# Performance work log

Hardware: AMD Instinct MI355X
Metric: run time of the kernel (lower is better)

Reference implementation:

```python
import jax, jax.numpy as jnp
import numpy as np

B, T, U, D, H, V = 2, 512, 128, 512, 512, 1024

def setup_inputs() -> dict:
    key = jax.random.key(0)
    k1, k2, k3, k4 = jax.random.split(key, 4)
    pred_inp = jax.random.normal(k1, (B, U, D), dtype=jnp.float32)
    enc_inp = jax.random.normal(k2, (B, T, D), dtype=jnp.float32)
    W0 = jax.random.normal(k3, (D, H), dtype=jnp.float32) * (1.0 / np.sqrt(D))
    b0 = jnp.zeros((H,), dtype=jnp.float32)
    W1 = jax.random.normal(k4, (H, V), dtype=jnp.float32) * (1.0 / np.sqrt(H))
    b1 = jnp.zeros((V,), dtype=jnp.float32)
    return {"pred_inp": pred_inp, "enc_inp": enc_inp, "W0": W0, "b0": b0, "W1": W1, "b1": b1}

def reference(pred_inp, enc_inp, W0, b0, W1, b1):
    # broadcast-add: enc [B,T,1,D] + pred [B,1,U,D] -> [B,T,U,D]
    x = enc_inp[:, :, None, :] + pred_inp[:, None, :, :]
    # Dense(additional_size)
    h = jnp.einsum('btud,dh->btuh', x, W0) + b0
    # Dense(output_size)
    out = jnp.einsum('btuh,hv->btuv', h, W1) + b1
    return out
```

## Files before the change

kernel.cpp:

```cpp
#include <hip/hip_runtime.h>


typedef float vf4 __attribute__((ext_vector_type(4)));
typedef short bf16x8 __attribute__((ext_vector_type(8)));
typedef float f32x4 __attribute__((ext_vector_type(4)));
typedef unsigned short us4 __attribute__((ext_vector_type(4)));

#define PADK 40

__device__ __forceinline__ unsigned short f2bf(float f) {
    union { float f; unsigned u; } v; v.f = f;
    const unsigned r = v.u + 0x7FFFu + ((v.u >> 16) & 1u);
    return (unsigned short)(r >> 16);
}

__global__ __launch_bounds__(256) void prep(
    const float* __restrict__ pred, const float* __restrict__ enc,
    const float* __restrict__ W0, const float* __restrict__ b0,
    const float* __restrict__ W1, const float* __restrict__ b1,
    unsigned short* __restrict__ xbf,
    unsigned short* __restrict__ WcT,
    float* __restrict__ bcv)
{
    __shared__ unsigned short As[64 * PADK];
    __shared__ unsigned short Bst[64 * PADK];
    __shared__ float b0s[512];

    const int bid = blockIdx.x;
    const int tid = threadIdx.x;

    if (bid < 128) {
        const int row0 = (bid >> 4) << 6;
        const int col0 = (bid & 15) << 6;
        const int w = tid >> 6, lane = tid & 63;
        const int l16 = lane & 15, kq = lane >> 4;

        float4 ar[2], br[2];
        auto loadA = [&](int kb) {
            #pragma unroll
            for (int i = 0; i < 2; ++i) {
                const int idx = tid + (i << 8);
                const int r = idx >> 3, k4 = (idx & 7) << 2;
                ar[i] = *reinterpret_cast<const float4*>(
                    W0 + (size_t)(row0 + r) * 512 + kb + k4);
            }
        };
        auto loadB = [&](int kb) {
            #pragma unroll
            for (int i = 0; i < 2; ++i) {
                const int idx = tid + (i << 8);
                const int kk = idx >> 4, n4 = (idx & 15) << 2;
                br[i] = *reinterpret_cast<const float4*>(
                    W1 + (size_t)(kb + kk) * 1024 + col0 + n4);
            }
        };
        auto stage = [&]() {
            #pragma unroll
            for (int i = 0; i < 2; ++i) {
                const int idx = tid + (i << 8);
                const int r = idx >> 3, k4 = (idx & 7) << 2;
                us4 p = { f2bf(ar[i].x), f2bf(ar[i].y), f2bf(ar[i].z), f2bf(ar[i].w) };
                *reinterpret_cast<us4*>(&As[r * PADK + k4]) = p;
                const int kk = idx >> 4, n4 = (idx & 15) << 2;
                Bst[(n4 + 0) * PADK + kk] = f2bf(br[i].x);
                Bst[(n4 + 1) * PADK + kk] = f2bf(br[i].y);
                Bst[(n4 + 2) * PADK + kk] = f2bf(br[i].z);
                Bst[(n4 + 3) * PADK + kk] = f2bf(br[i].w);
            }
        };

        f32x4 acc[4] = {};
        loadA(0); loadB(0);
        for (int kt = 0; kt < 16; ++kt) {
            __syncthreads();
            stage();
            __syncthreads();
            if (kt < 15) { loadA((kt + 1) << 5); loadB((kt + 1) << 5); }
            bf16x8 a = *reinterpret_cast<const bf16x8*>(&As[(w * 16 + l16) * PADK + kq * 8]);
            #pragma unroll
            for (int nf = 0; nf < 4; ++nf) {
                bf16x8 b = *reinterpret_cast<const bf16x8*>(&Bst[(nf * 16 + l16) * PADK + kq * 8]);
                acc[nf] = __builtin_amdgcn_mfma_f32_16x16x32_bf16(a, b, acc[nf], 0, 0, 0);
            }
        }
        const int cr0 = row0 + w * 16 + kq * 4;
        #pragma unroll
        for (int nf = 0; nf < 4; ++nf) {
            const int c = col0 + nf * 16 + l16;
            us4 p = { f2bf(acc[nf][0]), f2bf(acc[nf][1]),
                      f2bf(acc[nf][2]), f2bf(acc[nf][3]) };
            *reinterpret_cast<us4*>(&WcT[(size_t)c * 512 + cr0]) = p;
        }
    } else if (bid < 448) {
        const int i = ((bid - 128) << 8) + tid;
        const int r = i >> 6;
        const int k8 = (i & 63) << 3;
        const float* src = (r < 1024)
            ? enc + (size_t)r * 512 + k8
            : pred + (size_t)(r - 1024) * 512 + k8;
        const float4 a = *reinterpret_cast<const float4*>(src);
        const float4 c = *reinterpret_cast<const float4*>(src + 4);
        us4 p0 = { f2bf(a.x), f2bf(a.y), f2bf(a.z), f2bf(a.w) };
        us4 p1 = { f2bf(c.x), f2bf(c.y), f2bf(c.z), f2bf(c.w) };
        *reinterpret_cast<us4*>(&xbf[(size_t)r * 512 + k8]) = p0;
        *reinterpret_cast<us4*>(&xbf[(size_t)r * 512 + k8 + 4]) = p1;
    } else {
        for (int i = tid; i < 512; i += 256) b0s[i] = b0[i];
        __syncthreads();
        const int v = ((bid - 448) << 8) + tid;
        float acc = b1[v];
        #pragma unroll 8
        for (int h = 0; h < 512; ++h)
            acc = fmaf(b0s[h], W1[(size_t)h * 1024 + v], acc);
        bcv[v] = acc;
    }
}

__global__ __launch_bounds__(256) void gemm_y(
    const unsigned short* __restrict__ xbf,
    const unsigned short* __restrict__ WcT,
    const float* __restrict__ bcv,
    float* __restrict__ Q)
{
    __shared__ unsigned short As[2][64 * PADK];
    __shared__ unsigned short Bs[2][64 * PADK];

    const int tid = threadIdx.x;
    const int row0 = blockIdx.y << 6;
    const int col0 = blockIdx.x << 6;
    const int w = tid >> 6, lane = tid & 63;
    const int l16 = lane & 15, kq = lane >> 4;
    const int sr = tid >> 2, sk8 = (tid & 3) << 3;

    const unsigned short* Arow = xbf + (size_t)(row0 + sr) * 512 + sk8;
    const unsigned short* Brow = WcT + (size_t)(col0 + sr) * 512 + sk8;

    bf16x8 areg, breg;
    auto loadg = [&](int kb) {
        areg = *reinterpret_cast<const bf16x8*>(Arow + kb);
        breg = *reinterpret_cast<const bf16x8*>(Brow + kb);
    };
    auto stage = [&](int buf) {
        *reinterpret_cast<bf16x8*>(&As[buf][sr * PADK + sk8]) = areg;
        *reinterpret_cast<bf16x8*>(&Bs[buf][sr * PADK + sk8]) = breg;
    };

    f32x4 acc[4] = {};
    loadg(0);
    stage(0);
    __syncthreads();
    int buf = 0;
    for (int kt = 0; kt < 16; ++kt) {
        if (kt < 15) loadg((kt + 1) << 5);
        bf16x8 a = *reinterpret_cast<const bf16x8*>(&As[buf][(w * 16 + l16) * PADK + kq * 8]);
        #pragma unroll
        for (int nf = 0; nf < 4; ++nf) {
            bf16x8 b = *reinterpret_cast<const bf16x8*>(&Bs[buf][(nf * 16 + l16) * PADK + kq * 8]);
            acc[nf] = __builtin_amdgcn_mfma_f32_16x16x32_bf16(a, b, acc[nf], 0, 0, 0);
        }
        if (kt < 15) stage(buf ^ 1);
        __syncthreads();
        buf ^= 1;
    }

    const int cr0 = row0 + w * 16 + kq * 4;
    const bool doBias = (row0 >= 1024);
    #pragma unroll
    for (int nf = 0; nf < 4; ++nf) {
        const int c = col0 + nf * 16 + l16;
        const float bv = doBias ? bcv[c] : 0.0f;
        #pragma unroll
        for (int r = 0; r < 4; ++r)
            Q[(size_t)(cr0 + r) * 1024 + c] = acc[nf][r] + bv;
    }
}

__global__ __launch_bounds__(256) void bcast_add(
    const vf4* __restrict__ Q, vf4* __restrict__ out)
{
    const int bid = blockIdx.x;
    const int g   = bid >> 4;
    const int uh  = (bid >> 3) & 1;
    const int vt  = bid & 7;
    const int bt0 = g << 3;
    const int b   = bt0 >> 9;
    const int u8  = threadIdx.x >> 5;
    const int c4  = threadIdx.x & 31;
    const int vcol = vt * 32 + c4;

    vf4 ye[8], yp[8];
    #pragma unroll
    for (int i = 0; i < 8; ++i)
        ye[i] = Q[(size_t)(bt0 + i) * 256 + vcol];
    const int urow0 = 1024 + b * 128 + uh * 64 + u8 * 8;
    #pragma unroll
    for (int i = 0; i < 8; ++i)
        yp[i] = Q[(size_t)(urow0 + i) * 256 + vcol];

    #pragma unroll
    for (int bt = 0; bt < 8; ++bt) {
        vf4* o = out + ((size_t)(bt0 + bt) * 128 + uh * 64 + u8 * 8) * 256 + vcol;
        #pragma unroll
        for (int uu = 0; uu < 8; ++uu) {
            __builtin_nontemporal_store(ye[bt] + yp[uu], o + (size_t)uu * 256);
        }
    }
}

extern "C" void kernel_launch(void* const* d_in, const int* in_sizes, int n_in,
                              void* d_out, int out_size, void* d_ws, size_t ws_size,
                              hipStream_t stream)
{
    const float* pred = (const float*)d_in[0];
    const float* enc  = (const float*)d_in[1];
    const float* W0   = (const float*)d_in[2];
    const float* b0   = (const float*)d_in[3];
    const float* W1   = (const float*)d_in[4];
    const float* b1   = (const float*)d_in[5];
    float* out = (float*)d_out;

    char* base = (char*)d_ws;
    unsigned short* xbf = (unsigned short*)base;
    unsigned short* WcT = (unsigned short*)(base + (2 << 20));
    float* bcv          = (float*)(base + (4 << 20));
    float* Q            = (float*)(base + (8 << 20));

    prep<<<452, 256, 0, stream>>>(pred, enc, W0, b0, W1, b1, xbf, WcT, bcv);

    gemm_y<<<dim3(16, 20), 256, 0, stream>>>(xbf, WcT, bcv, Q);

    bcast_add<<<2048, 256, 0, stream>>>((const vf4*)Q, (vf4*)out);
}
```

Measured before the change: 128.3 us.

## Project enc/pred through W0 first instead of precomputing fused W0·W1 weight

```diff
diff --git a/kernel.cpp b/kernel.cpp
--- a/kernel.cpp
+++ b/kernel.cpp
@@ -17,21 +17,20 @@
 __global__ __launch_bounds__(256) void prep(
     const float* __restrict__ pred, const float* __restrict__ enc,
     const float* __restrict__ W0, const float* __restrict__ b0,
-    const float* __restrict__ W1, const float* __restrict__ b1,
-    unsigned short* __restrict__ xbf,
-    unsigned short* __restrict__ WcT,
-    float* __restrict__ bcv)
+    const float* __restrict__ W1,
+    unsigned short* __restrict__ P,
+    unsigned short* __restrict__ W1T)
 {
     __shared__ unsigned short As[64 * PADK];
     __shared__ unsigned short Bst[64 * PADK];
-    __shared__ float b0s[512];
+    __shared__ unsigned short Tr[64 * 68];
 
     const int bid = blockIdx.x;
     const int tid = threadIdx.x;
 
-    if (bid < 128) {
-        const int row0 = (bid >> 4) << 6;
-        const int col0 = (bid & 15) << 6;
+    if (bid < 160) {
+        const int tn = bid & 7, tm = bid >> 3;
+        const int row0 = tm << 6, col0 = tn << 6;
         const int w = tid >> 6, lane = tid & 63;
         const int l16 = lane & 15, kq = lane >> 4;
 
@@ -41,8 +40,10 @@
             for (int i = 0; i < 2; ++i) {
                 const int idx = tid + (i << 8);
                 const int r = idx >> 3, k4 = (idx & 7) << 2;
-                ar[i] = *reinterpret_cast<const float4*>(
-                    W0 + (size_t)(row0 + r) * 512 + kb + k4);
+                const float* Arow = (row0 < 1024)
+                    ? enc + (size_t)(row0 + r) * 512
+                    : pred + (size_t)(row0 - 1024 + r) * 512;
+                ar[i] = *reinterpret_cast<const float4*>(Arow + kb + k4);
             }
         };
         auto loadB = [&](int kb) {
@@ -51,7 +52,7 @@
                 const int idx = tid + (i << 8);
                 const int kk = idx >> 4, n4 = (idx & 15) << 2;
                 br[i] = *reinterpret_cast<const float4*>(
-                    W1 + (size_t)(kb + kk) * 1024 + col0 + n4);
+                    W0 + (size_t)(kb + kk) * 512 + col0 + n4);
             }
         };
         auto stage = [&]() {
@@ -84,42 +85,50 @@
             }
         }
         const int cr0 = row0 + w * 16 + kq * 4;
+        const bool doBias = (row0 >= 1024);
         #pragma unroll
         for (int nf = 0; nf < 4; ++nf) {
             const int c = col0 + nf * 16 + l16;
-            us4 p = { f2bf(acc[nf][0]), f2bf(acc[nf][1]),
-                      f2bf(acc[nf][2]), f2bf(acc[nf][3]) };
-            *reinterpret_cast<us4*>(&WcT[(size_t)c * 512 + cr0]) = p;
-        }
-    } else if (bid < 448) {
-        const int i = ((bid - 128) << 8) + tid;
-        const int r = i >> 6;
-        const int k8 = (i & 63) << 3;
-        const float* src = (r < 1024)
-            ? enc + (size_t)r * 512 + k8
-            : pred + (size_t)(r - 1024) * 512 + k8;
-        const float4 a = *reinterpret_cast<const float4*>(src);
-        const float4 c = *reinterpret_cast<const float4*>(src + 4);
-        us4 p0 = { f2bf(a.x), f2bf(a.y), f2bf(a.z), f2bf(a.w) };
-        us4 p1 = { f2bf(c.x), f2bf(c.y), f2bf(c.z), f2bf(c.w) };
-        *reinterpret_cast<us4*>(&xbf[(size_t)r * 512 + k8]) = p0;
-        *reinterpret_cast<us4*>(&xbf[(size_t)r * 512 + k8 + 4]) = p1;
+            const float bv = doBias ? b0[c] : 0.0f;
+            #pragma unroll
+            for (int r = 0; r < 4; ++r)
+                P[(size_t)(cr0 + r) * 512 + c] = f2bf(acc[nf][r] + bv);
+        }
     } else {
-        for (int i = tid; i < 512; i += 256) b0s[i] = b0[i];
+        const int t  = bid - 160;
+        const int kt = t >> 4;
+        const int nt = t & 15;
+        const int k0 = kt << 6, n0 = nt << 6;
+
+        {
+            const int r = tid >> 2, c0 = (tid & 3) << 4;
+            const float* src = W1 + (size_t)(k0 + r) * 1024 + n0 + c0;
+            #pragma unroll
+            for (int j = 0; j < 4; ++j) {
+                const float4 v = *reinterpret_cast<const float4*>(src + (j << 2));
+                const int c = c0 + (j << 2);
+                Tr[(c + 0) * 68 + r] = f2bf(v.x);
+                Tr[(c + 1) * 68 + r] = f2bf(v.y);
+                Tr[(c + 2) * 68 + r] = f2bf(v.z);
+                Tr[(c + 3) * 68 + r] = f2bf(v.w);
+            }
+        }
         __syncthreads();
-        const int v = ((bid - 448) << 8) + tid;
-        float acc = b1[v];
-        #pragma unroll 8
-        for (int h = 0; h < 512; ++h)
-            acc = fmaf(b0s[h], W1[(size_t)h * 1024 + v], acc);
-        bcv[v] = acc;
+        {
+            const int rr = tid >> 2, k8 = (tid & 3) << 4;
+            unsigned short* dst = W1T + (size_t)(n0 + rr) * 512 + k0 + k8;
+            *reinterpret_cast<bf16x8*>(dst) =
+                *reinterpret_cast<const bf16x8*>(&Tr[rr * 68 + k8]);
+            *reinterpret_cast<bf16x8*>(dst + 8) =
+                *reinterpret_cast<const bf16x8*>(&Tr[rr * 68 + k8 + 8]);
+        }
     }
 }
 
 __global__ __launch_bounds__(256) void gemm_y(
-    const unsigned short* __restrict__ xbf,
-    const unsigned short* __restrict__ WcT,
-    const float* __restrict__ bcv,
+    const unsigned short* __restrict__ P,
+    const unsigned short* __restrict__ W1T,
+    const float* __restrict__ b1,
     float* __restrict__ Q)
 {
     __shared__ unsigned short As[2][64 * PADK];
@@ -132,8 +141,8 @@
     const int l16 = lane & 15, kq = lane >> 4;
     const int sr = tid >> 2, sk8 = (tid & 3) << 3;
 
-    const unsigned short* Arow = xbf + (size_t)(row0 + sr) * 512 + sk8;
-    const unsigned short* Brow = WcT + (size_t)(col0 + sr) * 512 + sk8;
+    const unsigned short* Arow = P + (size_t)(row0 + sr) * 512 + sk8;
+    const unsigned short* Brow = W1T + (size_t)(col0 + sr) * 512 + sk8;
 
     bf16x8 areg, breg;
     auto loadg = [&](int kb) {
@@ -168,7 +177,7 @@
     #pragma unroll
     for (int nf = 0; nf < 4; ++nf) {
         const int c = col0 + nf * 16 + l16;
-        const float bv = doBias ? bcv[c] : 0.0f;
+        const float bv = doBias ? b1[c] : 0.0f;
         #pragma unroll
         for (int r = 0; r < 4; ++r)
             Q[(size_t)(cr0 + r) * 1024 + c] = acc[nf][r] + bv;
@@ -220,14 +229,13 @@
     float* out = (float*)d_out;
 
     char* base = (char*)d_ws;
-    unsigned short* xbf = (unsigned short*)base;
-    unsigned short* WcT = (unsigned short*)(base + (2 << 20));
-    float* bcv          = (float*)(base + (4 << 20));
-    float* Q            = (float*)(base + (8 << 20));
-
-    prep<<<452, 256, 0, stream>>>(pred, enc, W0, b0, W1, b1, xbf, WcT, bcv);
-
-    gemm_y<<<dim3(16, 20), 256, 0, stream>>>(xbf, WcT, bcv, Q);
+    unsigned short* P   = (unsigned short*)base;
+    unsigned short* W1T = (unsigned short*)(base + (2 << 20));
+    float* Q            = (float*)(base + (4 << 20));
+
+    prep<<<288, 256, 0, stream>>>(pred, enc, W0, b0, W1, P, W1T);
+
+    gemm_y<<<dim3(16, 20), 256, 0, stream>>>(P, W1T, b1, Q);
 
     bcast_add<<<2048, 256, 0, stream>>>((const vf4*)Q, (vf4*)out);
 }
```

After: 114.9 us. -10.4%, faster.
